# Kernel optimization log

Measured on AMD Instinct MI355X. Metric: run time of the kernel, lower is better.

## Reference

```python
import jax, jax.numpy as jnp
import numpy as np

VERTS = [5023, 1256, 314, 79, 20]
SPIRAL_LEN = 9
T_FRAMES = 32
LATENT = 64


def _spiral_conv(x, idx, W, b):
    # x: [B, N, C]; idx: [N, L]; gather spiral neighborhoods then linear
    B = x.shape[0]
    g = x[:, idx.reshape(-1), :].reshape(B, idx.shape[0], -1)  # [B, N, L*C]
    return g @ W.T + b


def _pool(x, rows, cols, vals, n_out):
    # sparse matmul: out[b, rows] += x[b, cols] * vals  (index_select + scatter_add)
    gathered = x[:, cols, :] * vals[None, :, None]
    return jnp.zeros((x.shape[0], n_out, x.shape[2]), x.dtype).at[:, rows, :].add(gathered)


def _lstm_dir(x, Wih, Whh, bih, bhh, reverse):
    # x: [T, B, D]; PyTorch gate order i, f, g, o
    Bz, H = x.shape[1], Whh.shape[1]
    bias = bih + bhh
    def step(carry, xt):
        h, c = carry
        g = xt @ Wih.T + h @ Whh.T + bias
        i, f, gg, o = jnp.split(g, 4, axis=-1)
        c = jax.nn.sigmoid(f) * c + jax.nn.sigmoid(i) * jnp.tanh(gg)
        h = jax.nn.sigmoid(o) * jnp.tanh(c)
        return (h, c), h
    init = (jnp.zeros((Bz, H), x.dtype), jnp.zeros((Bz, H), x.dtype))
    _, hs = jax.lax.scan(step, init, x, reverse=reverse)
    return hs


def _forward(audio_hidden, vertices, actor,
             sp_idx0, sp_idx1, sp_idx2, sp_idx3,
             d0_rows, d0_cols, d0_vals, d1_rows, d1_cols, d1_vals,
             d2_rows, d2_cols, d2_vals, d3_rows, d3_cols, d3_vals,
             u0_rows, u0_cols, u0_vals, u1_rows, u1_cols, u1_vals,
             u2_rows, u2_cols, u2_vals, u3_rows, u3_cols, u3_vals,
             enc_W0, enc_b0, enc_W1, enc_b1, enc_W2, enc_b2, enc_W3, enc_b3,
             enc_lin_W, enc_lin_b, dec_lin_W, dec_lin_b,
             dec_W0, dec_b0, dec_W1, dec_b1, dec_W2, dec_b2, dec_W3, dec_b3,
             dec_W4, dec_b4, aud_W, aud_b,
             l0_Wih, l0_Whh, l0_bih, l0_bhh, l12_Wih, l12_Whh, l12_bih, l12_bhh):
    ah = audio_hidden
    if ah.shape[1] % 2 != 0:
        ah = ah[:, :ah.shape[1] - 1]
    tv = vertices.shape[1]
    if ah.shape[1] > 2 * tv:
        ah = ah[:, :2 * tv]
    elif ah.shape[1] < 2 * tv:
        tv = ah.shape[1] // 2
    hs = ah.reshape(1, ah.shape[1] // 2, ah.shape[2] * 2)[:, :tv]  # [1, T, 1536]
    audio_emb = hs @ aud_W.T + aud_b                                # [1, T, LATENT]
    # --- mesh encoder on actor template: (spiral conv -> ELU -> down pool) x4 -> Linear ---
    sp = (sp_idx0, sp_idx1, sp_idx2, sp_idx3)
    down = ((d0_rows, d0_cols, d0_vals), (d1_rows, d1_cols, d1_vals),
            (d2_rows, d2_cols, d2_vals), (d3_rows, d3_cols, d3_vals))
    encp = ((enc_W0, enc_b0), (enc_W1, enc_b1), (enc_W2, enc_b2), (enc_W3, enc_b3))
    x = actor
    for i in range(4):
        x = jax.nn.elu(_spiral_conv(x, sp[i], *encp[i]))
        x = _pool(x, *down[i], VERTS[i + 1])
    z = x.reshape(x.shape[0], -1) @ enc_lin_W.T + enc_lin_b        # [1, LATENT]
    actor_emb = jnp.broadcast_to(z[:, None, :], audio_emb.shape)
    # --- 3-layer bidirectional LSTM ---
    h = jnp.concatenate([audio_emb, actor_emb], axis=-1).transpose(1, 0, 2)  # [T, 1, 2*LATENT]
    for layer in range(3):
        if layer == 0:
            Wih, Whh, bih, bhh = l0_Wih, l0_Whh, l0_bih, l0_bhh
        else:
            Wih, Whh, bih, bhh = l12_Wih[layer - 1], l12_Whh[layer - 1], l12_bih[layer - 1], l12_bhh[layer - 1]
        f = _lstm_dir(h, Wih[0], Whh[0], bih[0], bhh[0], False)
        r = _lstm_dir(h, Wih[1], Whh[1], bih[1], bhh[1], True)
        h = jnp.concatenate([f, r], axis=-1)
    latent = h.transpose(1, 0, 2)[0]                               # [T, LATENT]
    # --- mesh decoder, batched over all frames (replaces the python per-frame loop) ---
    up = ((u0_rows, u0_cols, u0_vals), (u1_rows, u1_cols, u1_vals),
          (u2_rows, u2_cols, u2_vals), (u3_rows, u3_cols, u3_vals))
    decp = ((dec_W0, dec_b0), (dec_W1, dec_b1), (dec_W2, dec_b2), (dec_W3, dec_b3))
    y = latent @ dec_lin_W.T + dec_lin_b                           # [T, 20*256]
    y = y.reshape(y.shape[0], VERTS[4], -1)                        # [T, 20, 256]
    for i in range(4):
        j = 3 - i
        y = _pool(y, *up[j], VERTS[j])
        y = jax.nn.elu(_spiral_conv(y, sp[j], *decp[i]))
    y = _spiral_conv(y, sp[0], dec_W4, dec_b4)                     # [T, 5023, 3]
    return y + actor                                               # broadcast residual, == vstacked preds


def setup_inputs() -> dict:
    key = jax.random.key(0)
    ks = iter(jax.random.split(key, 96))
    def nrm(shape, s=0.05):
        return jax.random.normal(next(ks), shape, jnp.float32) * s
    def rint(shape, hi):
        return jax.random.randint(next(ks), shape, 0, hi)
    inp = {}
    inp['audio_hidden'] = nrm((1, 2 * T_FRAMES, 768), 1.0)
    inp['vertices'] = nrm((1, T_FRAMES, VERTS[0], 3), 1.0)
    inp['actor'] = nrm((1, VERTS[0], 3), 1.0)
    for i in range(4):
        inp['sp_idx%d' % i] = rint((VERTS[i], SPIRAL_LEN), VERTS[i])
    for i in range(4):
        nnz = 3 * VERTS[i + 1]
        inp['d%d_rows' % i] = rint((nnz,), VERTS[i + 1])
        inp['d%d_cols' % i] = rint((nnz,), VERTS[i])
        inp['d%d_vals' % i] = jax.random.uniform(next(ks), (nnz,), jnp.float32)
    for i in range(4):
        nnz = 3 * VERTS[i]
        inp['u%d_rows' % i] = rint((nnz,), VERTS[i])
        inp['u%d_cols' % i] = rint((nnz,), VERTS[i + 1])
        inp['u%d_vals' % i] = jax.random.uniform(next(ks), (nnz,), jnp.float32)
    OC = [32, 64, 128, 256]
    ic = 3
    for i in range(4):
        inp['enc_W%d' % i] = nrm((OC[i], ic * SPIRAL_LEN))
        inp['enc_b%d' % i] = nrm((OC[i],))
        ic = OC[i]
    inp['enc_lin_W'] = nrm((LATENT, VERTS[4] * OC[3]))
    inp['enc_lin_b'] = nrm((LATENT,))
    inp['dec_lin_W'] = nrm((VERTS[4] * OC[3], LATENT))
    inp['dec_lin_b'] = nrm((VERTS[4] * OC[3],))
    dic = [256, 256, 128, 64]
    doc = [256, 128, 64, 32]
    for i in range(4):
        inp['dec_W%d' % i] = nrm((doc[i], dic[i] * SPIRAL_LEN))
        inp['dec_b%d' % i] = nrm((doc[i],))
    inp['dec_W4'] = nrm((3, OC[0] * SPIRAL_LEN))
    inp['dec_b4'] = nrm((3,))
    inp['aud_W'] = nrm((LATENT, 1536))
    inp['aud_b'] = nrm((LATENT,))
    H = LATENT // 2
    inp['l0_Wih'] = nrm((2, 4 * H, 2 * LATENT))
    inp['l0_Whh'] = nrm((2, 4 * H, H))
    inp['l0_bih'] = nrm((2, 4 * H))
    inp['l0_bhh'] = nrm((2, 4 * H))
    inp['l12_Wih'] = nrm((2, 2, 4 * H, 2 * H))
    inp['l12_Whh'] = nrm((2, 2, 4 * H, H))
    inp['l12_bih'] = nrm((2, 2, 4 * H))
    inp['l12_bhh'] = nrm((2, 2, 4 * H))
    return inp


def reference(audio_hidden, vertices, actor,
              sp_idx0, sp_idx1, sp_idx2, sp_idx3,
              d0_rows, d0_cols, d0_vals, d1_rows, d1_cols, d1_vals,
              d2_rows, d2_cols, d2_vals, d3_rows, d3_cols, d3_vals,
              u0_rows, u0_cols, u0_vals, u1_rows, u1_cols, u1_vals,
              u2_rows, u2_cols, u2_vals, u3_rows, u3_cols, u3_vals,
              enc_W0, enc_b0, enc_W1, enc_b1, enc_W2, enc_b2, enc_W3, enc_b3,
              enc_lin_W, enc_lin_b, dec_lin_W, dec_lin_b,
              dec_W0, dec_b0, dec_W1, dec_b1, dec_W2, dec_b2, dec_W3, dec_b3,
              dec_W4, dec_b4, aud_W, aud_b,
              l0_Wih, l0_Whh, l0_bih, l0_bhh, l12_Wih, l12_Whh, l12_bih, l12_bhh):
    return _forward(audio_hidden, vertices, actor,
                    sp_idx0, sp_idx1, sp_idx2, sp_idx3,
                    d0_rows, d0_cols, d0_vals, d1_rows, d1_cols, d1_vals,
                    d2_rows, d2_cols, d2_vals, d3_rows, d3_cols, d3_vals,
                    u0_rows, u0_cols, u0_vals, u1_rows, u1_cols, u1_vals,
                    u2_rows, u2_cols, u2_vals, u3_rows, u3_cols, u3_vals,
                    enc_W0, enc_b0, enc_W1, enc_b1, enc_W2, enc_b2, enc_W3, enc_b3,
                    enc_lin_W, enc_lin_b, dec_lin_W, dec_lin_b,
                    dec_W0, dec_b0, dec_W1, dec_b1, dec_W2, dec_b2, dec_W3, dec_b3,
                    dec_W4, dec_b4, aud_W, aud_b,
                    l0_Wih, l0_Whh, l0_bih, l0_bhh, l12_Wih, l12_Whh, l12_bih, l12_bhh)
```

## Files before the change

kernel.cpp:

```cpp
#include <hip/hip_runtime.h>
#include <cstdint>
#include <cstddef>


typedef unsigned short u16;
typedef __attribute__((ext_vector_type(8))) short short8;
typedef __attribute__((ext_vector_type(4))) float float4v;
#define CDIV(a,b) (((a)+(b)-1)/(b))
#define POOL_CAP 64

__device__ __forceinline__ float bf(u16 u){ return __uint_as_float(((unsigned)u)<<16); }
__device__ __forceinline__ u16 fb(float x){
  unsigned u = __float_as_uint(x);
  unsigned r = u + 0x7fffu + ((u>>16)&1u);
  return (u16)(r>>16);
}
__device__ __forceinline__ float lo16(unsigned u){ return __uint_as_float(u<<16); }
__device__ __forceinline__ float hi16(unsigned u){ return __uint_as_float(u & 0xffff0000u); }

struct WCast { const float* src[7]; int cum[8]; };
struct Lists {
  const int* rows[8];
  int nnz[8];
  int curoff[8];
  int lstoff[8];
};

__global__ void __launch_bounds__(256) setup_k(
    Lists L, int totN, int NF, int* __restrict__ curBase, int* __restrict__ lstBase,
    WCast C, int totW, int NC, u16* __restrict__ Wbf,
    const float* __restrict__ audio, const float* __restrict__ audW,
    const float* __restrict__ audB, float* __restrict__ h0,
    const float* __restrict__ actor, const int* __restrict__ sp0,
    const float* __restrict__ encW0, const float* __restrict__ encB0,
    u16* __restrict__ outA){
  int blk = blockIdx.x;
  int tid = threadIdx.x;
  if (blk < NF){
    int i = blk*256 + tid;
    if (i < totN){
      int off = i, k = 0;
      while (off >= L.nnz[k]){ off -= L.nnz[k]; k++; }
      int r = L.rows[k][off];
      int p = atomicAdd(curBase + L.curoff[k] + r, 1);
      if (p < POOL_CAP) lstBase[L.lstoff[k] + r*POOL_CAP + p] = off;
    }
    return;
  }
  blk -= NF;
  if (blk < NC){
    int i = blk*256 + tid;
    if (i < totW){
      int k = 0;
      while (i >= C.cum[k+1]) k++;
      Wbf[i] = fb(C.src[k][i - C.cum[k]]);
    }
    return;
  }
  blk -= NC;
  if (blk < 32){
    int t = blk;
    int f = tid >> 2, sl = tid & 3;
    const float4* x4 = (const float4*)(audio + t*1536);
    const float4* w4 = (const float4*)(audW + f*1536);
    float acc = 0.f;
    for (int k=sl; k<384; k+=4){
      float4 xv = x4[k], wv = w4[k];
      acc += xv.x*wv.x + xv.y*wv.y + xv.z*wv.z + xv.w*wv.w;
    }
    acc += __shfl_down(acc, 2, 64);
    acc += __shfl_down(acc, 1, 64);
    if (sl == 0) h0[t*128 + f] = acc + audB[f];
    return;
  }
  blk -= 32;
  int i = blk*256 + tid;
  if (i >= 5023*32) return;
  int o = i % 32; int v = i / 32;
  const float* wrow = encW0 + (size_t)o*27;
  const int* vix = sp0 + v*9;
  float acc = encB0[o];
  for (int s=0;s<9;s++){
    const float* xr = actor + (size_t)vix[s]*3;
    acc += xr[0]*wrow[s*3] + xr[1]*wrow[s*3+1] + xr[2]*wrow[s*3+2];
  }
  if (acc < 0.f) acc = expm1f(acc);
  outA[i] = fb(acc);
}

template<int IC, int BN, int BM>
__global__ void __launch_bounds__(256) conv_mfma(
    const u16* __restrict__ x, const int* __restrict__ idx,
    const u16* __restrict__ Wb, const float* __restrict__ bias,
    u16* __restrict__ out, int V, int OC, int M){
  constexpr int K = 9*IC;
  constexpr int KC = K/32;
  constexpr int NT = BN/16;
  constexpr int MT = BM/64;
  constexpr int LOG2 = (IC==32?5: IC==64?6: IC==128?7:8);
  constexpr int AST = 40;
  __shared__ u16 Asm[2][BM*AST];
  __shared__ u16 Bsm[2][BN*AST];
  __shared__ int rowB[BM], rowV[BM];
  __shared__ int sidx[BM*9];
  int t = threadIdx.x;
  int m0 = blockIdx.x*BM;
  int o0 = blockIdx.y*BN;
  if (t < BM){
    int mg = m0 + t;
    if (mg < M){ int b = mg / V; rowB[t] = b; rowV[t] = mg - b*V; }
    else rowB[t] = -1;
  }
  __syncthreads();
  for (int i=t; i<BM*9; i+=256){
    int r = i/9, s = i - r*9;
    sidx[i] = (rowB[r] >= 0) ? idx[rowV[r]*9 + s] : 0;
  }
  int lane = t & 63, wave = t >> 6;
  int quad = lane >> 4, col = lane & 15;
  float4v acc[MT][NT];
  #pragma unroll
  for (int mi=0;mi<MT;mi++)
    #pragma unroll
    for (int nt=0;nt<NT;nt++) acc[mi][nt] = (float4v)0.f;

  uint4 aval[MT]; uint4 bval;
  auto fetch = [&](int kc){
    int s  = (kc*32) >> LOG2;
    int c0 = (kc*32) & (IC-1);
    #pragma unroll
    for (int rpt=0; rpt<MT; ++rpt){
      int seg = t + 256*rpt;
      int arow = seg >> 2, aq = seg & 3;
      int b = rowB[arow];
      uint4 v = {0u,0u,0u,0u};
      if (b >= 0){
        int ix = sidx[arow*9 + s];
        v = *(const uint4*)(x + ((size_t)b*V + ix)*IC + c0 + aq*8);
      }
      aval[rpt] = v;
    }
    if (t < BN*4){
      int br = t >> 2, bq = t & 3;
      bval = *(const uint4*)(Wb + (size_t)(o0+br)*K + kc*32 + bq*8);
    }
  };

  __syncthreads();
  fetch(0);

  for (int kc = 0; kc < KC; ++kc){
    int buf = kc & 1;
    #pragma unroll
    for (int rpt=0; rpt<MT; ++rpt){
      int seg = t + 256*rpt;
      int arow = seg >> 2, aq = seg & 3;
      *(uint4*)&Asm[buf][arow*AST + aq*8] = aval[rpt];
    }
    if (t < BN*4){
      int br = t >> 2, bq = t & 3;
      *(uint4*)&Bsm[buf][br*AST + bq*8] = bval;
    }
    __syncthreads();
    if (kc+1 < KC) fetch(kc+1);
    short8 a[MT];
    #pragma unroll
    for (int mi=0;mi<MT;mi++)
      a[mi] = *(const short8*)&Asm[buf][(wave*MT*16 + mi*16 + col)*AST + quad*8];
    #pragma unroll
    for (int nt=0; nt<NT; ++nt){
      short8 bfr = *(const short8*)&Bsm[buf][(nt*16 + col)*AST + quad*8];
      #pragma unroll
      for (int mi=0;mi<MT;mi++)
        acc[mi][nt] = __builtin_amdgcn_mfma_f32_16x16x32_bf16(a[mi], bfr, acc[mi][nt], 0, 0, 0);
    }
  }
  #pragma unroll
  for (int mi=0;mi<MT;mi++){
    #pragma unroll
    for (int nt=0; nt<NT; ++nt){
      int o = o0 + nt*16 + col;
      float bv = bias[o];
      #pragma unroll
      for (int r=0;r<4;r++){
        int mg = m0 + wave*MT*16 + mi*16 + quad*4 + r;
        if (mg < M){
          float val = acc[mi][nt][r] + bv;
          if (val < 0.f) val = expm1f(val);
          out[(size_t)mg*OC + o] = fb(val);
        }
      }
    }
  }
}

__global__ void pool_g8_k(const u16* __restrict__ x, const int* __restrict__ cols,
                          const float* __restrict__ vals, const int* __restrict__ cur,
                          const int* __restrict__ lst, u16* __restrict__ out,
                          int B, int Vin, int Vout, int C){
  int C8 = C >> 3;
  int total = B*Vout*C8;
  int i = blockIdx.x*blockDim.x + threadIdx.x;
  if (i >= total) return;
  int c8 = i % C8; int tt = i / C8; int r = tt % Vout; int b = tt / Vout;
  int deg = cur[r]; if (deg > POOL_CAP) deg = POOL_CAP;
  const int* le = lst + r*POOL_CAP;
  float a0=0.f,a1=0.f,a2=0.f,a3=0.f,a4=0.f,a5=0.f,a6=0.f,a7=0.f;
  for (int k=0;k<deg;k++){
    int e = le[k];
    float v = vals[e];
    uint4 xv = *(const uint4*)(x + ((size_t)b*Vin + (size_t)cols[e])*C + c8*8);
    a0 += v*lo16(xv.x); a1 += v*hi16(xv.x);
    a2 += v*lo16(xv.y); a3 += v*hi16(xv.y);
    a4 += v*lo16(xv.z); a5 += v*hi16(xv.z);
    a6 += v*lo16(xv.w); a7 += v*hi16(xv.w);
  }
  uint4 o;
  o.x = ((unsigned)fb(a0)) | (((unsigned)fb(a1))<<16);
  o.y = ((unsigned)fb(a2)) | (((unsigned)fb(a3))<<16);
  o.z = ((unsigned)fb(a4)) | (((unsigned)fb(a5))<<16);
  o.w = ((unsigned)fb(a6)) | (((unsigned)fb(a7))<<16);
  *(uint4*)(out + ((size_t)b*Vout + (size_t)r)*C + c8*8) = o;
}

__global__ void __launch_bounds__(256) enc_lin_k(
    const u16* __restrict__ x, const float* __restrict__ W,
    const float* __restrict__ b, float* __restrict__ h0){
  int f = blockIdx.x;
  int t = threadIdx.x;
  const ushort4* x4 = (const ushort4*)x;
  const float4* w4 = (const float4*)(W + (size_t)f*5120);
  float acc = 0.f;
  for (int k=t; k<1280; k+=256){
    ushort4 xv = x4[k]; float4 wv = w4[k];
    acc += bf(xv.x)*wv.x + bf(xv.y)*wv.y + bf(xv.z)*wv.z + bf(xv.w)*wv.w;
  }
  #pragma unroll
  for (int off=32; off; off>>=1) acc += __shfl_down(acc, off, 64);
  __shared__ float red[4];
  if ((t & 63) == 0) red[t>>6] = acc;
  __syncthreads();
  if (t < 32){
    float zf = b[f] + red[0] + red[1] + red[2] + red[3];
    h0[t*128 + 64 + f] = zf;
  }
}

__device__ __forceinline__ float sigm(float x){ return 1.f/(1.f+__expf(-x)); }
__device__ __forceinline__ float tanhfast(float x){ return 1.f - 2.f/(__expf(2.f*x)+1.f); }

__global__ void __launch_bounds__(256) lstm3_k(
    const float* __restrict__ h0,
    const float* __restrict__ l0_Wih, const float* __restrict__ l0_Whh,
    const float* __restrict__ l0_bih, const float* __restrict__ l0_bhh,
    const float* __restrict__ l12_Wih, const float* __restrict__ l12_Whh,
    const float* __restrict__ l12_bih, const float* __restrict__ l12_bhh,
    float* __restrict__ latent){
  __shared__ __align__(16) u16 xb[32*136];
  __shared__ __align__(16) float xp[2*32*128];
  __shared__ __align__(16) u16 obuf[32*64];
  __shared__ float bias_l[256];
  int t = threadIdx.x;
  int lane = t & 63, wave = t >> 6;
  int quad = lane >> 4, col = lane & 15;

  for (int i=t;i<32*128;i+=256){ int tt=i>>7, k=i&127; xb[tt*136+k]=fb(h0[i]); }

  for (int layer=0; layer<3; layer++){
    int IN = (layer==0)?128:64;
    const float *Wih,*Whh,*bih,*bhh;
    if (layer==0){ Wih=l0_Wih; Whh=l0_Whh; bih=l0_bih; bhh=l0_bhh; }
    else {
      int mb=(layer-1)*2;
      Wih=l12_Wih + (size_t)mb*128*64; Whh=l12_Whh + (size_t)mb*128*32;
      bih=l12_bih + mb*128; bhh=l12_bhh + mb*128;
    }
    bias_l[t] = bih[(t>>7)*128 + (t&127)] + bhh[(t>>7)*128 + (t&127)];
    __syncthreads();

    {
      int dirA = wave >> 1, o0 = (wave & 1)*64;
      const float* WA = Wih + (size_t)dirA*128*IN;
      float4v acc[2][4];
      #pragma unroll
      for (int mi=0;mi<2;mi++)
        #pragma unroll
        for (int nt=0;nt<4;nt++) acc[mi][nt] = (float4v)0.f;
      for (int kc=0; kc<IN/32; ++kc){
        short8 bfrag[4];
        #pragma unroll
        for (int nt=0;nt<4;nt++){
          const float* src = WA + (size_t)(o0+nt*16+col)*IN + kc*32 + quad*8;
          float4 w0 = *(const float4*)src;
          float4 w1 = *(const float4*)(src+4);
          alignas(16) u16 tmp[8] = {fb(w0.x),fb(w0.y),fb(w0.z),fb(w0.w),
                                    fb(w1.x),fb(w1.y),fb(w1.z),fb(w1.w)};
          bfrag[nt] = *(const short8*)tmp;
        }
        short8 afrag[2];
        #pragma unroll
        for (int mi=0;mi<2;mi++)
          afrag[mi] = *(const short8*)&xb[(mi*16+col)*136 + kc*32 + quad*8];
        #pragma unroll
        for (int nt=0;nt<4;nt++)
          #pragma unroll
          for (int mi=0;mi<2;mi++)
            acc[mi][nt] = __builtin_amdgcn_mfma_f32_16x16x32_bf16(afrag[mi], bfrag[nt], acc[mi][nt], 0, 0, 0);
      }
      #pragma unroll
      for (int mi=0;mi<2;mi++)
        #pragma unroll
        for (int nt=0;nt<4;nt++){
          int j = o0 + nt*16 + col;
          float bv = bias_l[dirA*128 + j];
          #pragma unroll
          for (int r=0;r<4;r++){
            int tt = mi*16 + quad*4 + r;
            xp[dirA*4096 + tt*128 + j] = acc[mi][nt][r] + bv;
          }
        }
    }
    __syncthreads();

    if (wave < 2){
      int dir = wave;
      bool rev = (dir == 1);
      int u = lane & 31, gp = lane >> 5;
      int jj0 = gp*64 + u;
      int jj1 = gp*64 + 32 + u;
      const float* W0 = Whh + (size_t)dir*128*32 + (size_t)jj0*32;
      const float* W1 = Whh + (size_t)dir*128*32 + (size_t)jj1*32;
      unsigned wa[16], wb[16];
      #pragma unroll
      for (int k=0;k<16;k++){
        float2 w0 = *(const float2*)&W0[2*k];
        float2 w1 = *(const float2*)&W1[2*k];
        wa[k] = ((unsigned)fb(w0.x)) | (((unsigned)fb(w0.y))<<16);
        wb[k] = ((unsigned)fb(w1.x)) | (((unsigned)fb(w1.y))<<16);
      }
      const float* xpd = xp + dir*4096;
      float xq0[32], xq1[32];
      #pragma unroll
      for (int s=0;s<32;s++){
        int tx = rev ? (31-s) : s;
        xq0[s] = xpd[tx*128 + jj0];
        xq1[s] = xpd[tx*128 + jj1];
      }
      float h[32];
      #pragma unroll
      for (int k=0;k<32;k++) h[k] = 0.f;
      float creg = 0.f;

      for (int s=0;s<32;s++){
        int tx = rev ? (31-s) : s;
        float g0 = xq0[s];
        float g1 = xq1[s];
        float p0=0.f,q0=0.f,p1=0.f,q1=0.f;
        #pragma unroll
        for (int k=0;k<16;k++){
          unsigned ua = wa[k], ub = wb[k];
          p0 = fmaf(h[2*k],   lo16(ua), p0);
          q0 = fmaf(h[2*k+1], hi16(ua), q0);
          p1 = fmaf(h[2*k],   lo16(ub), p1);
          q1 = fmaf(h[2*k+1], hi16(ub), q1);
        }
        g0 += p0 + q0;
        g1 += p1 + q1;
        float act0 = (gp == 1) ? tanhfast(g0) : sigm(g0);
        float act1 = sigm(g1);
        float gg = __shfl(act0, 32 + u, 64);
        float go = __shfl(act1, 32 + u, 64);
        float cn = act1*creg + act0*gg;
        float hn = go*tanhfast(cn);
        creg = (gp == 0) ? cn : 0.f;
        #pragma unroll
        for (int k=0;k<32;k++) h[k] = __shfl(hn, k, 64);
        if (gp == 0) obuf[tx*64 + dir*32 + u] = fb(hn);
      }
    }
    __syncthreads();
    if (layer < 2){
      for (int i=t;i<32*64;i+=256){ int tt=i>>6, k=i&63; xb[tt*136+k]=obuf[i]; }
      __syncthreads();
    }
  }
  for (int i=t;i<32*64;i+=256) latent[i] = bf(obuf[i]);
}

__global__ void dec_lin_k(const float* __restrict__ latent, const float* __restrict__ W,
                          const float* __restrict__ b, u16* __restrict__ y){
  int i = blockIdx.x*blockDim.x + threadIdx.x;
  if (i >= 32*5120) return;
  int r = i % 5120, t = i / 5120;
  const float4* x4 = (const float4*)(latent + t*64);
  const float4* w4 = (const float4*)(W + (size_t)r*64);
  float acc = b[r];
  #pragma unroll
  for (int k=0;k<16;k++){
    float4 xv=x4[k]; float4 wv=w4[k];
    acc += xv.x*wv.x+xv.y*wv.y+xv.z*wv.z+xv.w*wv.w;
  }
  y[i] = fb(acc);
}

__global__ void final_k(const u16* __restrict__ x, const int* __restrict__ idx,
                        const float* __restrict__ W, const float* __restrict__ bias,
                        const float* __restrict__ actor, float* __restrict__ out){
  __shared__ float Wsm[3*288];
  __shared__ float bsm[3];
  int t = threadIdx.x;
  for (int i=t;i<864;i+=256) Wsm[i]=W[i];
  if (t<3) bsm[t]=bias[t];
  __syncthreads();
  int g = blockIdx.x*256 + t;
  if (g >= 32*5023) return;
  int v = g % 5023, b = g / 5023;
  const u16* xb = x + (size_t)b*5023*32;
  const int* vix = idx + v*9;
  float a0=bsm[0], a1=bsm[1], a2=bsm[2];
  for (int s=0;s<9;s++){
    const ushort4* xr = (const ushort4*)(xb + (size_t)vix[s]*32);
    #pragma unroll
    for (int k=0;k<8;k++){
      ushort4 xv = xr[k];
      float x0=bf(xv.x), x1=bf(xv.y), x2=bf(xv.z), x3=bf(xv.w);
      int kk = s*32 + k*4;
      a0 += x0*Wsm[kk] + x1*Wsm[kk+1] + x2*Wsm[kk+2] + x3*Wsm[kk+3];
      a1 += x0*Wsm[288+kk] + x1*Wsm[288+kk+1] + x2*Wsm[288+kk+2] + x3*Wsm[288+kk+3];
      a2 += x0*Wsm[576+kk] + x1*Wsm[576+kk+1] + x2*Wsm[576+kk+2] + x3*Wsm[576+kk+3];
    }
  }
  out[(size_t)g*3+0] = a0 + actor[v*3+0];
  out[(size_t)g*3+1] = a1 + actor[v*3+1];
  out[(size_t)g*3+2] = a2 + actor[v*3+2];
}

extern "C" void kernel_launch(void* const* d_in, const int* in_sizes, int n_in,
                              void* d_out, int out_size, void* d_ws, size_t ws_size,
                              hipStream_t stream){
  (void)in_sizes; (void)n_in; (void)out_size; (void)ws_size;

  const float* audio = (const float*)d_in[0];
  const float* actor = (const float*)d_in[2];
  const int* sp[4]   = {(const int*)d_in[3],(const int*)d_in[4],(const int*)d_in[5],(const int*)d_in[6]};
  const int* drows[4]; const int* dcols[4]; const float* dvals[4];
  for (int i=0;i<4;i++){ drows[i]=(const int*)d_in[7+3*i]; dcols[i]=(const int*)d_in[8+3*i]; dvals[i]=(const float*)d_in[9+3*i]; }
  const int* urows[4]; const int* ucols[4]; const float* uvals[4];
  for (int i=0;i<4;i++){ urows[i]=(const int*)d_in[19+3*i]; ucols[i]=(const int*)d_in[20+3*i]; uvals[i]=(const float*)d_in[21+3*i]; }
  const float* encW[4]={(const float*)d_in[31],(const float*)d_in[33],(const float*)d_in[35],(const float*)d_in[37]};
  const float* encB[4]={(const float*)d_in[32],(const float*)d_in[34],(const float*)d_in[36],(const float*)d_in[38]};
  const float* enc_lin_W=(const float*)d_in[39]; const float* enc_lin_b=(const float*)d_in[40];
  const float* dec_lin_W=(const float*)d_in[41]; const float* dec_lin_b=(const float*)d_in[42];
  const float* decW[5]={(const float*)d_in[43],(const float*)d_in[45],(const float*)d_in[47],(const float*)d_in[49],(const float*)d_in[51]};
  const float* decB[5]={(const float*)d_in[44],(const float*)d_in[46],(const float*)d_in[48],(const float*)d_in[50],(const float*)d_in[52]};
  const float* audW=(const float*)d_in[53]; const float* audB=(const float*)d_in[54];
  const float* l0_Wih=(const float*)d_in[55]; const float* l0_Whh=(const float*)d_in[56];
  const float* l0_bih=(const float*)d_in[57]; const float* l0_bhh=(const float*)d_in[58];
  const float* l12_Wih=(const float*)d_in[59]; const float* l12_Whh=(const float*)d_in[60];
  const float* l12_bih=(const float*)d_in[61]; const float* l12_bhh=(const float*)d_in[62];
  float* out = (float*)d_out;

  char* base = (char*)d_ws;
  u16* A  = (u16*)base;
  u16* Bb = (u16*)(base + 10287104);
  int* curBase = (int*)(base + 30891520);
  int* lstBase = (int*)(base + 30924928);
  u16* Wbf = (u16*)(base + 33060224);
  float* sm = (float*)(base + 35788160);
  float* h0     = sm;
  float* latent = sm + 4096;

  const int wsz[7] = {64*288, 128*576, 256*1152, 256*2304, 128*2304, 64*1152, 32*576};
  WCast WC; int wcum = 0;
  const float* wsrc[7] = {encW[1],encW[2],encW[3],decW[0],decW[1],decW[2],decW[3]};
  int wo[7];
  for (int k=0;k<7;k++){ WC.src[k]=wsrc[k]; WC.cum[k]=wcum; wo[k]=wcum; wcum+=wsz[k]; }
  WC.cum[7]=wcum;

  const int pVout[8] = {1256,314,79,20,5023,1256,314,79};
  const int pNnz[8]  = {3768,942,237,60,15069,3768,942,237};
  Lists L; int curoff=0, lstoff=0, totnnz=0;
  const int* prow[8] = {drows[0],drows[1],drows[2],drows[3],urows[0],urows[1],urows[2],urows[3]};
  int curo[8], lsto[8];
  for (int k=0;k<8;k++){
    L.rows[k]=prow[k]; L.nnz[k]=pNnz[k];
    L.curoff[k]=curoff; L.lstoff[k]=lstoff;
    curo[k]=curoff; lsto[k]=lstoff;
    curoff += pVout[k]; lstoff += pVout[k]*POOL_CAP; totnnz += pNnz[k];
  }
  hipMemsetAsync(curBase, 0, (size_t)curoff*4, stream);

  int NF = CDIV(totnnz,256), NC = CDIV(wcum,256), NC3 = CDIV(5023*32,256);
  setup_k<<<NF+NC+32+NC3,256,0,stream>>>(L, totnnz, NF, curBase, lstBase,
                                         WC, wcum, NC, Wbf,
                                         audio, audW, audB, h0,
                                         actor, sp[0], encW[0], encB[0], A);

  pool_g8_k<<<CDIV(1256*4,256),256,0,stream>>>(A, dcols[0], dvals[0], curBase+curo[0], lstBase+lsto[0], Bb, 1, 5023, 1256, 32);
  conv_mfma<32,64,64><<<dim3(CDIV(1256,64),1),256,0,stream>>>(Bb, sp[1], Wbf+wo[0], encB[1], A, 1256, 64, 1256);
  pool_g8_k<<<CDIV(314*8,256),256,0,stream>>>(A, dcols[1], dvals[1], curBase+curo[1], lstBase+lsto[1], Bb, 1, 1256, 314, 64);
  conv_mfma<64,64,64><<<dim3(CDIV(314,64),2),256,0,stream>>>(Bb, sp[2], Wbf+wo[1], encB[2], A, 314, 128, 314);
  pool_g8_k<<<CDIV(79*16,256),256,0,stream>>>(A, dcols[2], dvals[2], curBase+curo[2], lstBase+lsto[2], Bb, 1, 314, 79, 128);
  conv_mfma<128,64,64><<<dim3(CDIV(79,64),4),256,0,stream>>>(Bb, sp[3], Wbf+wo[2], encB[3], A, 79, 256, 79);
  pool_g8_k<<<CDIV(20*32,256),256,0,stream>>>(A, dcols[3], dvals[3], curBase+curo[3], lstBase+lsto[3], Bb, 1, 79, 20, 256);

  enc_lin_k<<<64,256,0,stream>>>(Bb, enc_lin_W, enc_lin_b, h0);

  lstm3_k<<<1,256,0,stream>>>(h0, l0_Wih, l0_Whh, l0_bih, l0_bhh,
                              l12_Wih, l12_Whh, l12_bih, l12_bhh, latent);

  dec_lin_k<<<CDIV(32*5120,256),256,0,stream>>>(latent, dec_lin_W, dec_lin_b, A);

  pool_g8_k<<<CDIV(32*79*32,256),256,0,stream>>>(A, ucols[3], uvals[3], curBase+curo[7], lstBase+lsto[7], Bb, 32, 20, 79, 256);
  conv_mfma<256,64,64><<<dim3(CDIV(2528,64),4),256,0,stream>>>(Bb, sp[3], Wbf+wo[3], decB[0], A, 79, 256, 2528);

  pool_g8_k<<<CDIV(32*314*32,256),256,0,stream>>>(A, ucols[2], uvals[2], curBase+curo[6], lstBase+lsto[6], Bb, 32, 79, 314, 256);
  conv_mfma<256,64,64><<<dim3(CDIV(10048,64),2),256,0,stream>>>(Bb, sp[2], Wbf+wo[4], decB[1], A, 314, 128, 10048);

  pool_g8_k<<<CDIV(32*1256*16,256),256,0,stream>>>(A, ucols[1], uvals[1], curBase+curo[5], lstBase+lsto[5], Bb, 32, 314, 1256, 128);
  conv_mfma<128,64,128><<<dim3(CDIV(40192,128),1),256,0,stream>>>(Bb, sp[1], Wbf+wo[5], decB[2], A, 1256, 64, 40192);

  pool_g8_k<<<CDIV(32*5023*8,256),256,0,stream>>>(A, ucols[0], uvals[0], curBase+curo[4], lstBase+lsto[4], Bb, 32, 1256, 5023, 64);
  conv_mfma<64,32,128><<<dim3(CDIV(160736,128),1),256,0,stream>>>(Bb, sp[0], Wbf+wo[6], decB[3], A, 5023, 32, 160736);

  final_k<<<CDIV(32*5023,256),256,0,stream>>>(A, sp[0], decW[4], decB[4], actor, out);
}
```

Measured before the change: 592.8 us.

## Fuse encoder pooling into spiral conv gather and spread LSTM recurrence across all waves

Each encoder downsampling pool is folded into the next spiral convolution: the conv's A-tile fetch computes the sparse pooled row on the fly from the previous level's output, using a double-buffered LDS pipeline. This removes three pool launches and their intermediate round trips. The LSTM recurrence now runs on all 256 threads, one gate row per thread, with hidden state shared through LDS and a block barrier each step, in place of two waves doing register shuffles. The costs are redundant pooling work, since each pooled row is recomputed for every spiral neighbor that references it, and 32 block-wide syncs per layer.

Measured after the change: 756.3 us. 1.28x slower.

```diff
diff --git a/kernel.cpp b/kernel.cpp
--- a/kernel.cpp
+++ b/kernel.cpp
@@ -194,6 +194,99 @@
   }
 }
 
+template<int IC, int BN>
+__global__ void __launch_bounds__(256) conv_pool_mfma(
+    const u16* __restrict__ xprev, const int* __restrict__ idx,
+    const int* __restrict__ cols, const float* __restrict__ vals,
+    const int* __restrict__ cur, const int* __restrict__ lst,
+    const u16* __restrict__ Wb, const float* __restrict__ bias,
+    u16* __restrict__ out, int V, int OC, int M){
+  constexpr int K = 9*IC;
+  constexpr int KC = K/32;
+  constexpr int NT = BN/16;
+  constexpr int LOG2 = (IC==32?5: IC==64?6: IC==128?7:8);
+  constexpr int AST = 40;
+  __shared__ u16 Asm[2][64*AST];
+  __shared__ u16 Bsm[2][BN*AST];
+  __shared__ int sidx[64*9];
+  int t = threadIdx.x;
+  int m0 = blockIdx.x*64;
+  int o0 = blockIdx.y*BN;
+  for (int i=t; i<64*9; i+=256){
+    int r = i/9, s = i - r*9;
+    sidx[i] = (m0 + r < M) ? idx[(m0+r)*9 + s] : -1;
+  }
+  int lane = t & 63, wave = t >> 6;
+  int quad = lane >> 4, col = lane & 15;
+  float4v acc[NT];
+  #pragma unroll
+  for (int nt=0;nt<NT;nt++) acc[nt] = (float4v)0.f;
+
+  uint4 aval; uint4 bval;
+  int arow = t >> 2, aq = t & 3;
+  auto fetch = [&](int kc){
+    int s  = (kc*32) >> LOG2;
+    int c0 = (kc*32) & (IC-1);
+    int r = sidx[arow*9 + s];
+    float p0=0,p1=0,p2=0,p3=0,p4=0,p5=0,p6=0,p7=0;
+    if (r >= 0){
+      int deg = cur[r]; if (deg > POOL_CAP) deg = POOL_CAP;
+      const int* le = lst + r*POOL_CAP;
+      for (int e=0;e<deg;e++){
+        int ee = le[e];
+        float v = vals[ee];
+        uint4 xv = *(const uint4*)(xprev + (size_t)cols[ee]*IC + c0 + aq*8);
+        p0 = fmaf(v, lo16(xv.x), p0); p1 = fmaf(v, hi16(xv.x), p1);
+        p2 = fmaf(v, lo16(xv.y), p2); p3 = fmaf(v, hi16(xv.y), p3);
+        p4 = fmaf(v, lo16(xv.z), p4); p5 = fmaf(v, hi16(xv.z), p5);
+        p6 = fmaf(v, lo16(xv.w), p6); p7 = fmaf(v, hi16(xv.w), p7);
+      }
+    }
+    aval.x = ((unsigned)fb(p0)) | (((unsigned)fb(p1))<<16);
+    aval.y = ((unsigned)fb(p2)) | (((unsigned)fb(p3))<<16);
+    aval.z = ((unsigned)fb(p4)) | (((unsigned)fb(p5))<<16);
+    aval.w = ((unsigned)fb(p6)) | (((unsigned)fb(p7))<<16);
+    if (t < BN*4){
+      int br = t >> 2, bq = t & 3;
+      bval = *(const uint4*)(Wb + (size_t)(o0+br)*K + kc*32 + bq*8);
+    }
+  };
+
+  __syncthreads();
+  fetch(0);
+
+  for (int kc = 0; kc < KC; ++kc){
+    int buf = kc & 1;
+    *(uint4*)&Asm[buf][arow*AST + aq*8] = aval;
+    if (t < BN*4){
+      int br = t >> 2, bq = t & 3;
+      *(uint4*)&Bsm[buf][br*AST + bq*8] = bval;
+    }
+    __syncthreads();
+    if (kc+1 < KC) fetch(kc+1);
+    short8 a = *(const short8*)&Asm[buf][(wave*16 + col)*AST + quad*8];
+    #pragma unroll
+    for (int nt=0; nt<NT; ++nt){
+      short8 bfr = *(const short8*)&Bsm[buf][(nt*16 + col)*AST + quad*8];
+      acc[nt] = __builtin_amdgcn_mfma_f32_16x16x32_bf16(a, bfr, acc[nt], 0, 0, 0);
+    }
+  }
+  #pragma unroll
+  for (int nt=0; nt<NT; ++nt){
+    int o = o0 + nt*16 + col;
+    float bv = bias[o];
+    #pragma unroll
+    for (int r=0;r<4;r++){
+      int mg = m0 + wave*16 + quad*4 + r;
+      if (mg < M){
+        float val = acc[nt][r] + bv;
+        if (val < 0.f) val = expm1f(val);
+        out[(size_t)mg*OC + o] = fb(val);
+      }
+    }
+  }
+}
+
 __global__ void pool_g8_k(const u16* __restrict__ x, const int* __restrict__ cols,
                           const float* __restrict__ vals, const int* __restrict__ cur,
                           const int* __restrict__ lst, u16* __restrict__ out,
@@ -259,10 +352,16 @@
   __shared__ __align__(16) u16 xb[32*136];
   __shared__ __align__(16) float xp[2*32*128];
   __shared__ __align__(16) u16 obuf[32*64];
+  __shared__ __align__(16) u16 hsh[2][32];
   __shared__ float bias_l[256];
   int t = threadIdx.x;
   int lane = t & 63, wave = t >> 6;
   int quad = lane >> 4, col = lane & 15;
+  int dir = t >> 7;
+  bool rev = (dir == 1);
+  int w2 = (t >> 6) & 1;
+  int unit = w2*16 + col;
+  int jj = quad*32 + unit;
 
   for (int i=t;i<32*128;i+=256){ int tt=i>>7, k=i&127; xb[tt*136+k]=fb(h0[i]); }
 
@@ -275,7 +374,16 @@
       Wih=l12_Wih + (size_t)mb*128*64; Whh=l12_Whh + (size_t)mb*128*32;
       bih=l12_bih + mb*128; bhh=l12_bhh + mb*128;
     }
-    bias_l[t] = bih[(t>>7)*128 + (t&127)] + bhh[(t>>7)*128 + (t&127)];
+    const float* WhhD = Whh + (size_t)dir*128*32 + (size_t)jj*32;
+    unsigned whh[16];
+    #pragma unroll
+    for (int k=0;k<16;k++){
+      float2 w = *(const float2*)&WhhD[2*k];
+      whh[k] = ((unsigned)fb(w.x)) | (((unsigned)fb(w.y))<<16);
+    }
+    bias_l[t] = bih[dir*128 + (t&127)] + bhh[dir*128 + (t&127)];
+    if (quad == 0) hsh[dir][unit] = 0;
+    float creg = 0.f;
     __syncthreads();
 
     {
@@ -322,63 +430,40 @@
     }
     __syncthreads();
 
-    if (wave < 2){
-      int dir = wave;
-      bool rev = (dir == 1);
-      int u = lane & 31, gp = lane >> 5;
-      int jj0 = gp*64 + u;
-      int jj1 = gp*64 + 32 + u;
-      const float* W0 = Whh + (size_t)dir*128*32 + (size_t)jj0*32;
-      const float* W1 = Whh + (size_t)dir*128*32 + (size_t)jj1*32;
-      unsigned wa[16], wb[16];
+    for (int s=0;s<32;s++){
+      int tx = rev ? (31-s) : s;
+      float g = xp[dir*4096 + tx*128 + jj];
+      const uint4* h4 = (const uint4*)hsh[dir];
+      float a0=0.f,a1=0.f,a2=0.f,a3=0.f;
       #pragma unroll
-      for (int k=0;k<16;k++){
-        float2 w0 = *(const float2*)&W0[2*k];
-        float2 w1 = *(const float2*)&W1[2*k];
-        wa[k] = ((unsigned)fb(w0.x)) | (((unsigned)fb(w0.y))<<16);
-        wb[k] = ((unsigned)fb(w1.x)) | (((unsigned)fb(w1.y))<<16);
+      for (int k=0;k<4;k++){
+        uint4 hv = h4[k];
+        unsigned u0=whh[4*k], u1=whh[4*k+1], u2=whh[4*k+2], u3=whh[4*k+3];
+        a0 = fmaf(lo16(hv.x), lo16(u0), a0);
+        a0 = fmaf(hi16(hv.x), hi16(u0), a0);
+        a1 = fmaf(lo16(hv.y), lo16(u1), a1);
+        a1 = fmaf(hi16(hv.y), hi16(u1), a1);
+        a2 = fmaf(lo16(hv.z), lo16(u2), a2);
+        a2 = fmaf(hi16(hv.z), hi16(u2), a2);
+        a3 = fmaf(lo16(hv.w), lo16(u3), a3);
+        a3 = fmaf(hi16(hv.w), hi16(u3), a3);
       }
-      const float* xpd = xp + dir*4096;
-      float xq0[32], xq1[32];
-      #pragma unroll
-      for (int s=0;s<32;s++){
-        int tx = rev ? (31-s) : s;
-        xq0[s] = xpd[tx*128 + jj0];
-        xq1[s] = xpd[tx*128 + jj1];
+      g += (a0+a1) + (a2+a3);
+      float act = (quad == 2) ? tanhfast(g) : sigm(g);
+      float gi = __shfl(act, col, 64);
+      float gf = __shfl(act, 16+col, 64);
+      float gg = __shfl(act, 32+col, 64);
+      float go = __shfl(act, 48+col, 64);
+      if (quad == 0){
+        float cn = gf*creg + gi*gg;
+        float hn = go*tanhfast(cn);
+        creg = cn;
+        u16 hb = fb(hn);
+        hsh[dir][unit] = hb;
+        obuf[tx*64 + dir*32 + unit] = hb;
       }
-      float h[32];
-      #pragma unroll
-      for (int k=0;k<32;k++) h[k] = 0.f;
-      float creg = 0.f;
-
-      for (int s=0;s<32;s++){
-        int tx = rev ? (31-s) : s;
-        float g0 = xq0[s];
-        float g1 = xq1[s];
-        float p0=0.f,q0=0.f,p1=0.f,q1=0.f;
-        #pragma unroll
-        for (int k=0;k<16;k++){
-          unsigned ua = wa[k], ub = wb[k];
-          p0 = fmaf(h[2*k],   lo16(ua), p0);
-          q0 = fmaf(h[2*k+1], hi16(ua), q0);
-          p1 = fmaf(h[2*k],   lo16(ub), p1);
-          q1 = fmaf(h[2*k+1], hi16(ub), q1);
-        }
-        g0 += p0 + q0;
-        g1 += p1 + q1;
-        float act0 = (gp == 1) ? tanhfast(g0) : sigm(g0);
-        float act1 = sigm(g1);
-        float gg = __shfl(act0, 32 + u, 64);
-        float go = __shfl(act1, 32 + u, 64);
-        float cn = act1*creg + act0*gg;
-        float hn = go*tanhfast(cn);
-        creg = (gp == 0) ? cn : 0.f;
-        #pragma unroll
-        for (int k=0;k<32;k++) h[k] = __shfl(hn, k, 64);
-        if (gp == 0) obuf[tx*64 + dir*32 + u] = fb(hn);
-      }
-    }
-    __syncthreads();
+      __syncthreads();
+    }
     if (layer < 2){
       for (int i=t;i<32*64;i+=256){ int tt=i>>6, k=i&63; xb[tt*136+k]=obuf[i]; }
       __syncthreads();
@@ -496,15 +581,18 @@
                                          audio, audW, audB, h0,
                                          actor, sp[0], encW[0], encB[0], A);
 
-  pool_g8_k<<<CDIV(1256*4,256),256,0,stream>>>(A, dcols[0], dvals[0], curBase+curo[0], lstBase+lsto[0], Bb, 1, 5023, 1256, 32);
-  conv_mfma<32,64,64><<<dim3(CDIV(1256,64),1),256,0,stream>>>(Bb, sp[1], Wbf+wo[0], encB[1], A, 1256, 64, 1256);
-  pool_g8_k<<<CDIV(314*8,256),256,0,stream>>>(A, dcols[1], dvals[1], curBase+curo[1], lstBase+lsto[1], Bb, 1, 1256, 314, 64);
-  conv_mfma<64,64,64><<<dim3(CDIV(314,64),2),256,0,stream>>>(Bb, sp[2], Wbf+wo[1], encB[2], A, 314, 128, 314);
-  pool_g8_k<<<CDIV(79*16,256),256,0,stream>>>(A, dcols[2], dvals[2], curBase+curo[2], lstBase+lsto[2], Bb, 1, 314, 79, 128);
-  conv_mfma<128,64,64><<<dim3(CDIV(79,64),4),256,0,stream>>>(Bb, sp[3], Wbf+wo[2], encB[3], A, 79, 256, 79);
-  pool_g8_k<<<CDIV(20*32,256),256,0,stream>>>(A, dcols[3], dvals[3], curBase+curo[3], lstBase+lsto[3], Bb, 1, 79, 20, 256);
-
-  enc_lin_k<<<64,256,0,stream>>>(Bb, enc_lin_W, enc_lin_b, h0);
+  conv_pool_mfma<32,64><<<dim3(CDIV(1256,64),1),256,0,stream>>>(
+      A, sp[1], dcols[0], dvals[0], curBase+curo[0], lstBase+lsto[0],
+      Wbf+wo[0], encB[1], Bb, 1256, 64, 1256);
+  conv_pool_mfma<64,64><<<dim3(CDIV(314,64),2),256,0,stream>>>(
+      Bb, sp[2], dcols[1], dvals[1], curBase+curo[1], lstBase+lsto[1],
+      Wbf+wo[1], encB[2], A, 314, 128, 314);
+  conv_pool_mfma<128,64><<<dim3(CDIV(79,64),4),256,0,stream>>>(
+      A, sp[3], dcols[2], dvals[2], curBase+curo[2], lstBase+lsto[2],
+      Wbf+wo[2], encB[3], Bb, 79, 256, 79);
+  pool_g8_k<<<CDIV(20*32,256),256,0,stream>>>(Bb, dcols[3], dvals[3], curBase+curo[3], lstBase+lsto[3], A, 1, 79, 20, 256);
+
+  enc_lin_k<<<64,256,0,stream>>>(A, enc_lin_W, enc_lin_b, h0);
 
   lstm3_k<<<1,256,0,stream>>>(h0, l0_Wih, l0_Whh, l0_bih, l0_bhh,
                               l12_Wih, l12_Whh, l12_bih, l12_bhh, latent);
```

## Spread LSTM recurrence over all four waves with shared-memory hidden state

Applied to the files above, without the earlier changes.

The LSTM recurrent step now uses all 256 threads, with one gate row per thread and two waves per direction. Before, two waves each handled a direction with two gate rows per lane and 32 shuffles to broadcast h. The hidden state now goes through a small shared buffer in bf16, read as vectors, and the recurrent weights are loaded before the input-projection phase. This cuts per-thread serial FMA work and shuffles per step, but adds a block-wide __syncthreads on every timestep and rounds h to bf16 before it feeds back into the recurrence.

Measured after the change: 572.7 us (median of 2 runs). -3.4%, faster.

```diff
diff --git a/kernel.cpp b/kernel.cpp
--- a/kernel.cpp
+++ b/kernel.cpp
@@ -259,10 +259,16 @@
   __shared__ __align__(16) u16 xb[32*136];
   __shared__ __align__(16) float xp[2*32*128];
   __shared__ __align__(16) u16 obuf[32*64];
+  __shared__ __align__(16) u16 hsh[2][32];
   __shared__ float bias_l[256];
   int t = threadIdx.x;
   int lane = t & 63, wave = t >> 6;
   int quad = lane >> 4, col = lane & 15;
+  int dir = t >> 7;
+  bool rev = (dir == 1);
+  int w2 = (t >> 6) & 1;
+  int unit = w2*16 + col;
+  int jj = quad*32 + unit;
 
   for (int i=t;i<32*128;i+=256){ int tt=i>>7, k=i&127; xb[tt*136+k]=fb(h0[i]); }
 
@@ -275,7 +281,16 @@
       Wih=l12_Wih + (size_t)mb*128*64; Whh=l12_Whh + (size_t)mb*128*32;
       bih=l12_bih + mb*128; bhh=l12_bhh + mb*128;
     }
-    bias_l[t] = bih[(t>>7)*128 + (t&127)] + bhh[(t>>7)*128 + (t&127)];
+    const float* WhhD = Whh + (size_t)dir*128*32 + (size_t)jj*32;
+    unsigned whh[16];
+    #pragma unroll
+    for (int k=0;k<16;k++){
+      float2 w = *(const float2*)&WhhD[2*k];
+      whh[k] = ((unsigned)fb(w.x)) | (((unsigned)fb(w.y))<<16);
+    }
+    bias_l[t] = bih[dir*128 + (t&127)] + bhh[dir*128 + (t&127)];
+    if (quad == 0) hsh[dir][unit] = 0;
+    float creg = 0.f;
     __syncthreads();
 
     {
@@ -322,63 +337,40 @@
     }
     __syncthreads();
 
-    if (wave < 2){
-      int dir = wave;
-      bool rev = (dir == 1);
-      int u = lane & 31, gp = lane >> 5;
-      int jj0 = gp*64 + u;
-      int jj1 = gp*64 + 32 + u;
-      const float* W0 = Whh + (size_t)dir*128*32 + (size_t)jj0*32;
-      const float* W1 = Whh + (size_t)dir*128*32 + (size_t)jj1*32;
-      unsigned wa[16], wb[16];
+    for (int s=0;s<32;s++){
+      int tx = rev ? (31-s) : s;
+      float g = xp[dir*4096 + tx*128 + jj];
+      const uint4* h4 = (const uint4*)hsh[dir];
+      float a0=0.f,a1=0.f,a2=0.f,a3=0.f;
       #pragma unroll
-      for (int k=0;k<16;k++){
-        float2 w0 = *(const float2*)&W0[2*k];
-        float2 w1 = *(const float2*)&W1[2*k];
-        wa[k] = ((unsigned)fb(w0.x)) | (((unsigned)fb(w0.y))<<16);
-        wb[k] = ((unsigned)fb(w1.x)) | (((unsigned)fb(w1.y))<<16);
+      for (int k=0;k<4;k++){
+        uint4 hv = h4[k];
+        unsigned u0=whh[4*k], u1=whh[4*k+1], u2=whh[4*k+2], u3=whh[4*k+3];
+        a0 = fmaf(lo16(hv.x), lo16(u0), a0);
+        a0 = fmaf(hi16(hv.x), hi16(u0), a0);
+        a1 = fmaf(lo16(hv.y), lo16(u1), a1);
+        a1 = fmaf(hi16(hv.y), hi16(u1), a1);
+        a2 = fmaf(lo16(hv.z), lo16(u2), a2);
+        a2 = fmaf(hi16(hv.z), hi16(u2), a2);
+        a3 = fmaf(lo16(hv.w), lo16(u3), a3);
+        a3 = fmaf(hi16(hv.w), hi16(u3), a3);
       }
-      const float* xpd = xp + dir*4096;
-      float xq0[32], xq1[32];
-      #pragma unroll
-      for (int s=0;s<32;s++){
-        int tx = rev ? (31-s) : s;
-        xq0[s] = xpd[tx*128 + jj0];
-        xq1[s] = xpd[tx*128 + jj1];
+      g += (a0+a1) + (a2+a3);
+      float act = (quad == 2) ? tanhfast(g) : sigm(g);
+      float gi = __shfl(act, col, 64);
+      float gf = __shfl(act, 16+col, 64);
+      float gg = __shfl(act, 32+col, 64);
+      float go = __shfl(act, 48+col, 64);
+      if (quad == 0){
+        float cn = gf*creg + gi*gg;
+        float hn = go*tanhfast(cn);
+        creg = cn;
+        u16 hb = fb(hn);
+        hsh[dir][unit] = hb;
+        obuf[tx*64 + dir*32 + unit] = hb;
       }
-      float h[32];
-      #pragma unroll
-      for (int k=0;k<32;k++) h[k] = 0.f;
-      float creg = 0.f;
-
-      for (int s=0;s<32;s++){
-        int tx = rev ? (31-s) : s;
-        float g0 = xq0[s];
-        float g1 = xq1[s];
-        float p0=0.f,q0=0.f,p1=0.f,q1=0.f;
-        #pragma unroll
-        for (int k=0;k<16;k++){
-          unsigned ua = wa[k], ub = wb[k];
-          p0 = fmaf(h[2*k],   lo16(ua), p0);
-          q0 = fmaf(h[2*k+1], hi16(ua), q0);
-          p1 = fmaf(h[2*k],   lo16(ub), p1);
-          q1 = fmaf(h[2*k+1], hi16(ub), q1);
-        }
-        g0 += p0 + q0;
-        g1 += p1 + q1;
-        float act0 = (gp == 1) ? tanhfast(g0) : sigm(g0);
-        float act1 = sigm(g1);
-        float gg = __shfl(act0, 32 + u, 64);
-        float go = __shfl(act1, 32 + u, 64);
-        float cn = act1*creg + act0*gg;
-        float hn = go*tanhfast(cn);
-        creg = (gp == 0) ? cn : 0.f;
-        #pragma unroll
-        for (int k=0;k<32;k++) h[k] = __shfl(hn, k, 64);
-        if (gp == 0) obuf[tx*64 + dir*32 + u] = fb(hn);
-      }
-    }
-    __syncthreads();
+      __syncthreads();
+    }
     if (layer < 2){
       for (int i=t;i<32*64;i+=256){ int tt=i>>6, k=i&63; xb[tt*136+k]=obuf[i]; }
       __syncthreads();
```
